# Kernel optimization log

Hardware: AMD Instinct MI355X
Metric: run time of the kernel (lower is better)

## Reference

```python
import jax, jax.numpy as jnp
import numpy as np
from jax import lax

B, S, FEAT, OUT = 64, 8192, 8, 64


def setup_inputs() -> dict:
    key = jax.random.key(0)
    ks = jax.random.split(key, 7)
    x = jax.random.normal(ks[0], (B, S, FEAT), dtype=jnp.float32)
    # torch default init: U(-1/sqrt(fan_in), 1/sqrt(fan_in))
    def uinit(k, shape, fan_in):
        bound = 1.0 / np.sqrt(fan_in)
        return jax.random.uniform(k, shape, jnp.float32, -bound, bound)
    W1 = uinit(ks[1], (32, 1, 2, 2), 1 * 2 * 2)   # OIHW
    b1 = uinit(ks[2], (32,), 1 * 2 * 2)
    W2 = uinit(ks[3], (32, 32, 1, 2), 32 * 1 * 2)
    b2 = uinit(ks[4], (32,), 32 * 1 * 2)
    Wp = uinit(ks[5], (OUT, 64), 64)              # torch Linear: [out, in]
    bp = uinit(ks[6], (OUT,), 64)
    return {"x": x, "W1": W1, "b1": b1, "W2": W2, "b2": b2, "Wp": Wp, "bp": bp}


def reference(x, W1, b1, W2, b2, Wp, bp):
    b, s, _ = x.shape
    xg = x.reshape(b * s, 1, 2, 4)  # [N,1,2,4] NCHW
    dn = ("NCHW", "OIHW", "NCHW")
    h = lax.conv_general_dilated(xg, W1, (1, 1), "VALID", dimension_numbers=dn)
    h = jax.nn.relu(h + b1[None, :, None, None])          # [N,32,1,3]
    h = lax.conv_general_dilated(h, W2, (1, 1), "VALID", dimension_numbers=dn)
    h = jax.nn.relu(h + b2[None, :, None, None])          # [N,32,1,2]
    h = h.reshape(b * s, 64)                              # C*H*W flatten, matches torch
    out = h @ Wp.T + bp                                   # [N,64]
    return out.reshape(b, s, -1)
```

## Files before the change

### kernel.cpp

```cpp
#include <hip/hip_runtime.h>

typedef __attribute__((ext_vector_type(8))) __bf16 bf16x8;
typedef __attribute__((ext_vector_type(4))) float floatx4;

__device__ inline unsigned bf1(float a){
  unsigned u = __float_as_uint(a);
  return (u + 0x7FFFu + ((u >> 16) & 1u)) >> 16;
}
__device__ inline unsigned bfpack(float lo, float hi){
  return bf1(lo) | (bf1(hi) << 16);
}

#define LW2 0
#define LWP 2304
#define LA0 6912
#define LA1 11520
#define LH2 16128

__global__ __launch_bounds__(256) void cnn_fused(
    const float* __restrict__ x,  const float* __restrict__ W1,
    const float* __restrict__ b1, const float* __restrict__ W2,
    const float* __restrict__ b2, const float* __restrict__ Wp,
    const float* __restrict__ bp, float* __restrict__ out)
{
  __shared__ ushort lds[20736];
  unsigned* ldsu = (unsigned*)lds;
  const int tid = threadIdx.x;

  for (int i = tid; i < 2048; i += 256) lds[LW2 + (i >> 6)*72 + (i & 63)] = (ushort)bf1(W2[i]);
  for (int i = tid; i < 4096; i += 256) lds[LWP + (i >> 6)*72 + (i & 63)] = (ushort)bf1(Wp[i]);

  const int rowbase = blockIdx.x * 64;
  const int rl  = tid & 63;
  const int wid = tid >> 6;
  const long r = rowbase + rl;

  const float4 xa = ((const float4*)x)[2*r];
  const float4 xb = ((const float4*)x)[2*r + 1];

  #pragma unroll
  for (int i = 0; i < 8; ++i){
    const int oc = wid*8 + i;
    const float w00 = W1[oc*4+0], w01 = W1[oc*4+1];
    const float w10 = W1[oc*4+2], w11 = W1[oc*4+3];
    const float bb  = b1[oc];
    const float h0 = fmaxf(0.f, bb + w00*xa.x + w01*xa.y + w10*xb.x + w11*xb.y);
    const float h1 = fmaxf(0.f, bb + w00*xa.y + w01*xa.z + w10*xb.y + w11*xb.z);
    const float h2 = fmaxf(0.f, bb + w00*xa.z + w01*xa.w + w10*xb.z + w11*xb.w);
    ldsu[(LA0 + rl*72 + oc*2) >> 1] = bfpack(h0, h1);
    ldsu[(LA1 + rl*72 + oc*2) >> 1] = bfpack(h1, h2);
  }
  __syncthreads();

  const int lane = tid & 63, lm = lane & 15, quad = lane >> 4;
  const int arow = (wid*16 + lm)*72;

  bf16x8 a0k0 = *(const bf16x8*)&lds[LA0 + arow +      quad*8];
  bf16x8 a0k1 = *(const bf16x8*)&lds[LA0 + arow + 32 + quad*8];
  bf16x8 a1k0 = *(const bf16x8*)&lds[LA1 + arow +      quad*8];
  bf16x8 a1k1 = *(const bf16x8*)&lds[LA1 + arow + 32 + quad*8];

  bf16x8 b0k0 = *(const bf16x8*)&lds[LW2 + (lm)*72      +      quad*8];
  bf16x8 b0k1 = *(const bf16x8*)&lds[LW2 + (lm)*72      + 32 + quad*8];
  bf16x8 b1k0 = *(const bf16x8*)&lds[LW2 + (16+lm)*72   +      quad*8];
  bf16x8 b1k1 = *(const bf16x8*)&lds[LW2 + (16+lm)*72   + 32 + quad*8];

  floatx4 z = {0.f, 0.f, 0.f, 0.f};
  floatx4 acc00 = z, acc01 = z, acc10 = z, acc11 = z;
  acc00 = __builtin_amdgcn_mfma_f32_16x16x32_bf16(a0k0, b0k0, acc00, 0,0,0);
  acc00 = __builtin_amdgcn_mfma_f32_16x16x32_bf16(a0k1, b0k1, acc00, 0,0,0);
  acc01 = __builtin_amdgcn_mfma_f32_16x16x32_bf16(a0k0, b1k0, acc01, 0,0,0);
  acc01 = __builtin_amdgcn_mfma_f32_16x16x32_bf16(a0k1, b1k1, acc01, 0,0,0);
  acc10 = __builtin_amdgcn_mfma_f32_16x16x32_bf16(a1k0, b0k0, acc10, 0,0,0);
  acc10 = __builtin_amdgcn_mfma_f32_16x16x32_bf16(a1k1, b0k1, acc10, 0,0,0);
  acc11 = __builtin_amdgcn_mfma_f32_16x16x32_bf16(a1k0, b1k0, acc11, 0,0,0);
  acc11 = __builtin_amdgcn_mfma_f32_16x16x32_bf16(a1k1, b1k1, acc11, 0,0,0);

  const float b2a = b2[lm], b2b = b2[16 + lm];
  #pragma unroll
  for (int rg = 0; rg < 4; ++rg){
    const int m = wid*16 + quad*4 + rg;
    ldsu[(LH2 + m*72 + lm*2) >> 1] =
        bfpack(fmaxf(0.f, acc00[rg] + b2a), fmaxf(0.f, acc10[rg] + b2a));
    ldsu[(LH2 + m*72 + (16+lm)*2) >> 1] =
        bfpack(fmaxf(0.f, acc01[rg] + b2b), fmaxf(0.f, acc11[rg] + b2b));
  }
  __syncthreads();

  bf16x8 ca0 = *(const bf16x8*)&lds[LH2 + arow +      quad*8];
  bf16x8 ca1 = *(const bf16x8*)&lds[LH2 + arow + 32 + quad*8];

  floatx4 oacc[4];
  #pragma unroll
  for (int t = 0; t < 4; ++t){
    bf16x8 wb0 = *(const bf16x8*)&lds[LWP + (t*16+lm)*72 +      quad*8];
    bf16x8 wb1 = *(const bf16x8*)&lds[LWP + (t*16+lm)*72 + 32 + quad*8];
    floatx4 acc = z;
    acc = __builtin_amdgcn_mfma_f32_16x16x32_bf16(ca0, wb0, acc, 0,0,0);
    acc = __builtin_amdgcn_mfma_f32_16x16x32_bf16(ca1, wb1, acc, 0,0,0);
    oacc[t] = acc;
  }

  #pragma unroll
  for (int t = 0; t < 4; ++t){
    const float bpv = bp[t*16 + lm];
    #pragma unroll
    for (int rg = 0; rg < 4; ++rg){
      const int m = wid*16 + quad*4 + rg;
      out[(long)(rowbase + m)*64 + t*16 + lm] = oacc[t][rg] + bpv;
    }
  }
}

extern "C" void kernel_launch(void* const* d_in, const int* in_sizes, int n_in,
                              void* d_out, int out_size, void* d_ws, size_t ws_size,
                              hipStream_t stream)
{
  const float* x  = (const float*)d_in[0];
  const float* W1 = (const float*)d_in[1];
  const float* b1 = (const float*)d_in[2];
  const float* W2 = (const float*)d_in[3];
  const float* b2 = (const float*)d_in[4];
  const float* Wp = (const float*)d_in[5];
  const float* bp = (const float*)d_in[6];
  float* out = (float*)d_out;

  const int rows   = in_sizes[0] / 8;
  const int blocks = rows / 64;
  cnn_fused<<<blocks, 256, 0, stream>>>(x, W1, b1, W2, b2, Wp, bp, out);
}
```

Measured before the change: 188.4 us.

## Make kernel persistent with register-resident weights and per-wave tile loop

Switches from one block per 64 rows to a fixed grid of 1024 blocks where each wave loops over 16-row tiles. The W2 and Wp weight fragments are converted to bf16 once and kept in registers, so the per-block LDS weight staging disappears. Conv1 output is built directly in MFMA A-fragment layout in registers instead of passing through LDS. The next tile's input is prefetched during compute, and the output is written as float4 using a permuted Wp column order. The cost is higher register pressure, two block-wide syncs per iteration, and a tail that is dropped if the tile count does not divide evenly by the grid.

```diff
diff --git a/kernel.cpp b/kernel.cpp
--- a/kernel.cpp
+++ b/kernel.cpp
@@ -1,114 +1,138 @@
 #include <hip/hip_runtime.h>
 
 typedef __attribute__((ext_vector_type(8))) __bf16 bf16x8;
+typedef __attribute__((ext_vector_type(8))) ushort ushort8;
 typedef __attribute__((ext_vector_type(4))) float floatx4;
 
-__device__ inline unsigned bf1(float a){
+union FragU { ushort8 u; bf16x8 b; };
+
+__device__ inline ushort bf1(float a){
   unsigned u = __float_as_uint(a);
-  return (u + 0x7FFFu + ((u >> 16) & 1u)) >> 16;
+  return (ushort)((u + 0x7FFFu + ((u >> 16) & 1u)) >> 16);
 }
 __device__ inline unsigned bfpack(float lo, float hi){
-  return bf1(lo) | (bf1(hi) << 16);
+  return (unsigned)bf1(lo) | ((unsigned)bf1(hi) << 16);
 }
 
-#define LW2 0
-#define LWP 2304
-#define LA0 6912
-#define LA1 11520
-#define LH2 16128
+#define BLOCKS 1024
 
 __global__ __launch_bounds__(256) void cnn_fused(
     const float* __restrict__ x,  const float* __restrict__ W1,
     const float* __restrict__ b1, const float* __restrict__ W2,
     const float* __restrict__ b2, const float* __restrict__ Wp,
-    const float* __restrict__ bp, float* __restrict__ out)
+    const float* __restrict__ bp, float* __restrict__ out, int niter)
 {
-  __shared__ ushort lds[20736];
-  unsigned* ldsu = (unsigned*)lds;
-  const int tid = threadIdx.x;
+  __shared__ __align__(16) ushort h2buf[4 * 16 * 72];
+  const int tid  = threadIdx.x;
+  const int wid  = tid >> 6;
+  const int lane = tid & 63;
+  const int lm   = lane & 15;
+  const int quad = lane >> 4;
+  ushort*   myh2 = &h2buf[wid * (16 * 72)];
+  unsigned* h2d  = (unsigned*)myh2;
 
-  for (int i = tid; i < 2048; i += 256) lds[LW2 + (i >> 6)*72 + (i & 63)] = (ushort)bf1(W2[i]);
-  for (int i = tid; i < 4096; i += 256) lds[LWP + (i >> 6)*72 + (i & 63)] = (ushort)bf1(Wp[i]);
+  FragU w2f[2][2];
+  #pragma unroll
+  for (int t = 0; t < 2; ++t)
+    #pragma unroll
+    for (int h = 0; h < 2; ++h)
+      #pragma unroll
+      for (int j = 0; j < 8; ++j)
+        w2f[t][h].u[j] = bf1(W2[(t*16 + lm)*64 + (quad*8 + j)*2 + h]);
 
-  const int rowbase = blockIdx.x * 64;
-  const int rl  = tid & 63;
-  const int wid = tid >> 6;
-  const long r = rowbase + rl;
+  FragU wpf[4][2];
+  #pragma unroll
+  for (int t = 0; t < 4; ++t)
+    #pragma unroll
+    for (int h = 0; h < 2; ++h)
+      #pragma unroll
+      for (int j = 0; j < 8; ++j){
+        const int c   = h*32 + quad*8 + j;
+        const int cp  = c & 31;
+        const int oc2 = (cp >> 1) | ((cp & 1) << 4);
+        wpf[t][h].u[j] = bf1(Wp[(4*lm + t)*64 + oc2*2 + h]);
+      }
 
-  const float4 xa = ((const float4*)x)[2*r];
-  const float4 xb = ((const float4*)x)[2*r + 1];
-
+  float w1r[8][4], b1r[8];
   #pragma unroll
   for (int i = 0; i < 8; ++i){
-    const int oc = wid*8 + i;
-    const float w00 = W1[oc*4+0], w01 = W1[oc*4+1];
-    const float w10 = W1[oc*4+2], w11 = W1[oc*4+3];
-    const float bb  = b1[oc];
-    const float h0 = fmaxf(0.f, bb + w00*xa.x + w01*xa.y + w10*xb.x + w11*xb.y);
-    const float h1 = fmaxf(0.f, bb + w00*xa.y + w01*xa.z + w10*xb.y + w11*xb.z);
-    const float h2 = fmaxf(0.f, bb + w00*xa.z + w01*xa.w + w10*xb.z + w11*xb.w);
-    ldsu[(LA0 + rl*72 + oc*2) >> 1] = bfpack(h0, h1);
-    ldsu[(LA1 + rl*72 + oc*2) >> 1] = bfpack(h1, h2);
+    const int oc = quad*8 + i;
+    w1r[i][0] = W1[oc*4+0]; w1r[i][1] = W1[oc*4+1];
+    w1r[i][2] = W1[oc*4+2]; w1r[i][3] = W1[oc*4+3];
+    b1r[i]    = b1[oc];
   }
-  __syncthreads();
+  const float  b2a = b2[lm], b2b = b2[16 + lm];
+  const float4 bp4 = ((const float4*)bp)[lm];
 
-  const int lane = tid & 63, lm = lane & 15, quad = lane >> 4;
-  const int arow = (wid*16 + lm)*72;
+  const long gw   = (long)blockIdx.x * 4 + wid;
+  long tilebase   = gw * ((long)niter * 16);
 
-  bf16x8 a0k0 = *(const bf16x8*)&lds[LA0 + arow +      quad*8];
-  bf16x8 a0k1 = *(const bf16x8*)&lds[LA0 + arow + 32 + quad*8];
-  bf16x8 a1k0 = *(const bf16x8*)&lds[LA1 + arow +      quad*8];
-  bf16x8 a1k1 = *(const bf16x8*)&lds[LA1 + arow + 32 + quad*8];
+  const float4* x4 = (const float4*)x;
+  float4 xa = x4[2*(tilebase + lm)];
+  float4 xb = x4[2*(tilebase + lm) + 1];
 
-  bf16x8 b0k0 = *(const bf16x8*)&lds[LW2 + (lm)*72      +      quad*8];
-  bf16x8 b0k1 = *(const bf16x8*)&lds[LW2 + (lm)*72      + 32 + quad*8];
-  bf16x8 b1k0 = *(const bf16x8*)&lds[LW2 + (16+lm)*72   +      quad*8];
-  bf16x8 b1k1 = *(const bf16x8*)&lds[LW2 + (16+lm)*72   + 32 + quad*8];
+  const floatx4 z = {0.f, 0.f, 0.f, 0.f};
 
-  floatx4 z = {0.f, 0.f, 0.f, 0.f};
-  floatx4 acc00 = z, acc01 = z, acc10 = z, acc11 = z;
-  acc00 = __builtin_amdgcn_mfma_f32_16x16x32_bf16(a0k0, b0k0, acc00, 0,0,0);
-  acc00 = __builtin_amdgcn_mfma_f32_16x16x32_bf16(a0k1, b0k1, acc00, 0,0,0);
-  acc01 = __builtin_amdgcn_mfma_f32_16x16x32_bf16(a0k0, b1k0, acc01, 0,0,0);
-  acc01 = __builtin_amdgcn_mfma_f32_16x16x32_bf16(a0k1, b1k1, acc01, 0,0,0);
-  acc10 = __builtin_amdgcn_mfma_f32_16x16x32_bf16(a1k0, b0k0, acc10, 0,0,0);
-  acc10 = __builtin_amdgcn_mfma_f32_16x16x32_bf16(a1k1, b0k1, acc10, 0,0,0);
-  acc11 = __builtin_amdgcn_mfma_f32_16x16x32_bf16(a1k0, b1k0, acc11, 0,0,0);
-  acc11 = __builtin_amdgcn_mfma_f32_16x16x32_bf16(a1k1, b1k1, acc11, 0,0,0);
+  for (int it = 0; it < niter; ++it){
+    float4 nxa, nxb;
+    if (it + 1 < niter){
+      const long nr = tilebase + 16 + lm;
+      nxa = x4[2*nr]; nxb = x4[2*nr + 1];
+    }
 
-  const float b2a = b2[lm], b2b = b2[16 + lm];
-  #pragma unroll
-  for (int rg = 0; rg < 4; ++rg){
-    const int m = wid*16 + quad*4 + rg;
-    ldsu[(LH2 + m*72 + lm*2) >> 1] =
-        bfpack(fmaxf(0.f, acc00[rg] + b2a), fmaxf(0.f, acc10[rg] + b2a));
-    ldsu[(LH2 + m*72 + (16+lm)*2) >> 1] =
-        bfpack(fmaxf(0.f, acc01[rg] + b2b), fmaxf(0.f, acc11[rg] + b2b));
-  }
-  __syncthreads();
+    FragU F0, F1, F2;
+    #pragma unroll
+    for (int i = 0; i < 8; ++i){
+      const float w00 = w1r[i][0], w01 = w1r[i][1];
+      const float w10 = w1r[i][2], w11 = w1r[i][3], bb = b1r[i];
+      F0.u[i] = bf1(fmaxf(0.f, bb + w00*xa.x + w01*xa.y + w10*xb.x + w11*xb.y));
+      F1.u[i] = bf1(fmaxf(0.f, bb + w00*xa.y + w01*xa.z + w10*xb.y + w11*xb.z));
+      F2.u[i] = bf1(fmaxf(0.f, bb + w00*xa.z + w01*xa.w + w10*xb.z + w11*xb.w));
+    }
 
-  bf16x8 ca0 = *(const bf16x8*)&lds[LH2 + arow +      quad*8];
-  bf16x8 ca1 = *(const bf16x8*)&lds[LH2 + arow + 32 + quad*8];
+    floatx4 a00 = z, a01 = z, a10 = z, a11 = z;
+    a00 = __builtin_amdgcn_mfma_f32_16x16x32_bf16(F0.b, w2f[0][0].b, a00, 0,0,0);
+    a00 = __builtin_amdgcn_mfma_f32_16x16x32_bf16(F1.b, w2f[0][1].b, a00, 0,0,0);
+    a01 = __builtin_amdgcn_mfma_f32_16x16x32_bf16(F0.b, w2f[1][0].b, a01, 0,0,0);
+    a01 = __builtin_amdgcn_mfma_f32_16x16x32_bf16(F1.b, w2f[1][1].b, a01, 0,0,0);
+    a10 = __builtin_amdgcn_mfma_f32_16x16x32_bf16(F1.b, w2f[0][0].b, a10, 0,0,0);
+    a10 = __builtin_amdgcn_mfma_f32_16x16x32_bf16(F2.b, w2f[0][1].b, a10, 0,0,0);
+    a11 = __builtin_amdgcn_mfma_f32_16x16x32_bf16(F1.b, w2f[1][0].b, a11, 0,0,0);
+    a11 = __builtin_amdgcn_mfma_f32_16x16x32_bf16(F2.b, w2f[1][1].b, a11, 0,0,0);
 
-  floatx4 oacc[4];
-  #pragma unroll
-  for (int t = 0; t < 4; ++t){
-    bf16x8 wb0 = *(const bf16x8*)&lds[LWP + (t*16+lm)*72 +      quad*8];
-    bf16x8 wb1 = *(const bf16x8*)&lds[LWP + (t*16+lm)*72 + 32 + quad*8];
-    floatx4 acc = z;
-    acc = __builtin_amdgcn_mfma_f32_16x16x32_bf16(ca0, wb0, acc, 0,0,0);
-    acc = __builtin_amdgcn_mfma_f32_16x16x32_bf16(ca1, wb1, acc, 0,0,0);
-    oacc[t] = acc;
-  }
-
-  #pragma unroll
-  for (int t = 0; t < 4; ++t){
-    const float bpv = bp[t*16 + lm];
     #pragma unroll
     for (int rg = 0; rg < 4; ++rg){
-      const int m = wid*16 + quad*4 + rg;
-      out[(long)(rowbase + m)*64 + t*16 + lm] = oacc[t][rg] + bpv;
+      const int rr = (quad*4 + rg) * 36;
+      h2d[rr +      lm] = bfpack(fmaxf(0.f, a00[rg] + b2a), fmaxf(0.f, a01[rg] + b2b));
+      h2d[rr + 16 + lm] = bfpack(fmaxf(0.f, a10[rg] + b2a), fmaxf(0.f, a11[rg] + b2b));
     }
+    __syncthreads();
+
+    FragU ca0, ca1;
+    ca0.u = *(const ushort8*)&myh2[lm*72 +      quad*8];
+    ca1.u = *(const ushort8*)&myh2[lm*72 + 32 + quad*8];
+
+    floatx4 oacc[4];
+    #pragma unroll
+    for (int t = 0; t < 4; ++t){
+      floatx4 acc = z;
+      acc = __builtin_amdgcn_mfma_f32_16x16x32_bf16(ca0.b, wpf[t][0].b, acc, 0,0,0);
+      acc = __builtin_amdgcn_mfma_f32_16x16x32_bf16(ca1.b, wpf[t][1].b, acc, 0,0,0);
+      oacc[t] = acc;
+    }
+
+    #pragma unroll
+    for (int rg = 0; rg < 4; ++rg){
+      float4 v;
+      v.x = oacc[0][rg] + bp4.x;
+      v.y = oacc[1][rg] + bp4.y;
+      v.z = oacc[2][rg] + bp4.z;
+      v.w = oacc[3][rg] + bp4.w;
+      *(float4*)(out + (tilebase + quad*4 + rg)*64 + 4*lm) = v;
+    }
+    __syncthreads();
+
+    if (it + 1 < niter){ xa = nxa; xb = nxb; tilebase += 16; }
   }
 }
 
@@ -125,7 +149,8 @@
   const float* bp = (const float*)d_in[6];
   float* out = (float*)d_out;
 
-  const int rows   = in_sizes[0] / 8;
-  const int blocks = rows / 64;
-  cnn_fused<<<blocks, 256, 0, stream>>>(x, W1, b1, W2, b2, Wp, bp, out);
+  const int rows  = in_sizes[0] / 8;
+  const int tiles = rows / 16;
+  const int niter = tiles / (BLOCKS * 4);
+  cnn_fused<<<BLOCKS, 256, 0, stream>>>(x, W1, b1, W2, b2, Wp, bp, out, niter);
 }
```

Measured after the change: 180.3 us. -4.3%, faster.
